# Performance work log

Hardware: AMD Instinct MI355X
Metric: run time of the kernel (lower is better)

Reference implementation:

```python
import jax, jax.numpy as jnp
import numpy as np

NUM_NODE = 100000
B, L, D = 128, 50, 128
HOP = 2
S = 8            # n_sample
NEIGHBOR_N = 9   # FindNeighbors top-k
BETA = 0.005
LEAKY = 0.2      # opt.alpha


def _local_agg(h, adj, a_local):
    # h: [B,N,D], adj: [B,N,N] int with edge types 0..4, a_local: [4,D]
    # e_k[b,i,j] = leakyrelu(sum_d h[b,i,d]*h[b,j,d]*a_k[d]) without [B,N,N,D] blowup
    e = jnp.stack([jnp.einsum('bid,bjd->bij', h * a_local[k], h) for k in range(4)])
    e = jax.nn.leaky_relu(e, LEAKY)
    att = jnp.full(e.shape[1:], -9e15, dtype=h.dtype)
    for k in range(4):
        att = jnp.where(adj == k + 1, e[k], att)
    att = jax.nn.softmax(att, axis=-1)
    return att @ h


def _global_agg(self_v, neigh_v, neigh_w, extra, w1, w2, w3):
    # self_v [B,M,D], neigh_v [B,M,S,D], neigh_w [B,M,S], extra (session info) [B,M,D]
    x = jnp.concatenate([extra[:, :, None, :] * neigh_v, neigh_w[..., None]], axis=-1)  # [B,M,S,D+1]
    alpha = jax.nn.leaky_relu(jnp.einsum('bmse,ed->bmsd', x, w1), LEAKY)
    alpha = jax.nn.softmax(jnp.einsum('bmsd,d->bms', alpha, w2[:, 0]), axis=-1)
    neigh = jnp.sum(alpha[..., None] * neigh_v, axis=-2)                                # [B,M,D]
    out = jnp.concatenate([self_v, neigh], axis=-1) @ w3
    return jax.nn.relu(out)


def _ssl(h_local, h_global):
    b, l, _ = h_local.shape
    kr, kc = jax.random.split(jax.random.key(42))
    corrupted = h_local[jax.random.permutation(kr, b)][:, jax.random.permutation(kc, l)]
    pos = jnp.sum(h_local * h_global, axis=1)
    neg = jnp.sum(h_global * corrupted, axis=1)
    return jnp.sum(-jnp.log(1e-8 + jax.nn.sigmoid(pos))
                   - jnp.log(1e-8 + 1.0 - jax.nn.sigmoid(neg)))


def _compute_scores(hidden, mask, pos_embedding, w1, w2, glu1_w, glu1_b, glu2_w, embedding):
    b, l, d = hidden.shape
    m = mask.astype(hidden.dtype)[..., None]                       # [B,L,1]
    pos = jnp.broadcast_to(pos_embedding[:l][None], hidden.shape)  # [B,L,D]
    hs = jnp.sum(hidden * m, axis=1) / jnp.sum(m, axis=1)          # [B,D]
    nh = jnp.tanh(jnp.concatenate([pos, hidden], axis=-1) @ w1)
    ns = jax.nn.sigmoid(nh @ glu1_w.T + glu1_b + hs[:, None, :] @ glu2_w.T)
    beta = (ns @ w2) * m                                           # [B,L,1]
    select = jnp.sum(beta * hidden, axis=1)                        # [B,D]
    # FindNeighbors: top-k cosine-similarity attention across the batch
    norm = jnp.sqrt(jnp.sum(select * select + 1e-6, axis=1))[:, None]
    cos = jax.nn.softmax((select @ select.T) / (norm @ norm.T), axis=-1)
    k = min(NEIGHBOR_N, b)
    topv, topi = jax.lax.top_k(cos, k)
    topv = jax.nn.softmax(topv, axis=-1)
    neighbor = jnp.sum(topv[..., None] * select[topi], axis=1)     # [B,D]
    select = select + neighbor                                     # dropout40: eval identity
    return select @ embedding[1:].T                                # [B, num_node-1]


def _forward(inputs, adj, mask_item, item, adj_all, num_w, embedding, pos_embedding,
             a_local, gw1, gw2, gw3, w1, w2, glu1_w, glu1_b, glu2_w):
    b, l = inputs.shape
    d = embedding.shape[1]
    h = embedding[inputs]
    h_local = _local_agg(h, adj, a_local)
    # multi-hop neighbor sampling via global adjacency table
    item_neighbors = [inputs]
    weight_neighbors = []
    support = l
    for _ in range(HOP):
        flat = item_neighbors[-1].reshape(-1)
        support *= S
        item_neighbors.append(adj_all[flat].reshape(b, support))
        weight_neighbors.append(num_w[flat].reshape(b, support))
    entity = [embedding[x] for x in item_neighbors]
    mf = mask_item.astype(h.dtype)
    item_emb = embedding[item] * mf[..., None]
    sess = jnp.sum(item_emb, axis=1) / jnp.sum(mf, axis=-1)[:, None]   # [B,D]
    session_info = [jnp.broadcast_to(sess[:, None, :], ev.shape) for ev in entity[:HOP]]
    for n_hop in range(HOP):
        nxt = []
        for i in range(HOP - n_hop):
            nv = entity[i + 1].reshape(b, -1, S, d)
            nw = weight_neighbors[i].reshape(b, -1, S)
            nxt.append(_global_agg(entity[i], nv, nw, session_info[i],
                                   gw1[n_hop], gw2[n_hop], gw3[n_hop]))
        entity = nxt
    h_global = entity[0].reshape(b, l, d)
    output = h_local + h_global  # dropout_local/global: eval identity
    con_loss = _ssl(h_local, h_global)
    scores = _compute_scores(output, mask_item, pos_embedding, w1, w2,
                             glu1_w, glu1_b, glu2_w, embedding)
    return output, BETA * con_loss, scores


def setup_inputs() -> dict:
    key = jax.random.key(0)
    ks = jax.random.split(key, 18)
    s = 0.08  # ~ uniform(-1/sqrt(D), 1/sqrt(D)) scale
    return {
        'inputs': jax.random.randint(ks[0], (B, L), 0, NUM_NODE, dtype=jnp.int32),
        'adj': jax.random.randint(ks[1], (B, L, L), 0, 5, dtype=jnp.int32),
        'mask_item': jax.random.randint(ks[2], (B, L), 0, 2, dtype=jnp.int32).at[:, 0].set(1),
        'item': jax.random.randint(ks[3], (B, L), 0, NUM_NODE, dtype=jnp.int32),
        'targets': jax.random.randint(ks[4], (B,), 0, NUM_NODE, dtype=jnp.int32),
        'adj_all': jax.random.randint(ks[5], (NUM_NODE, S), 0, NUM_NODE, dtype=jnp.int32),
        'num_w': jax.random.uniform(ks[6], (NUM_NODE, S), dtype=jnp.float32),
        'embedding': jax.random.normal(ks[7], (NUM_NODE, D), dtype=jnp.float32) * s,
        'pos_embedding': jax.random.normal(ks[8], (200, D), dtype=jnp.float32) * s,
        'a_local': jax.random.normal(ks[9], (4, D), dtype=jnp.float32) * s,
        'gw1': jax.random.normal(ks[10], (HOP, D + 1, D), dtype=jnp.float32) * s,
        'gw2': jax.random.normal(ks[11], (HOP, D, 1), dtype=jnp.float32) * s,
        'gw3': jax.random.normal(ks[12], (HOP, 2 * D, D), dtype=jnp.float32) * s,
        'w1': jax.random.normal(ks[13], (2 * D, D), dtype=jnp.float32) * s,
        'w2': jax.random.normal(ks[14], (D, 1), dtype=jnp.float32) * s,
        'glu1_w': jax.random.normal(ks[15], (D, D), dtype=jnp.float32) * s,
        'glu1_b': jax.random.normal(ks[16], (D,), dtype=jnp.float32) * s,
        'glu2_w': jax.random.normal(ks[17], (D, D), dtype=jnp.float32) * s,
    }


def reference(inputs, adj, mask_item, item, targets, adj_all, num_w, embedding,
              pos_embedding, a_local, gw1, gw2, gw3, w1, w2, glu1_w, glu1_b, glu2_w):
    # targets embedding lookup in the original is dead code (targets1 unused)
    return _forward(inputs, adj, mask_item, item, adj_all, num_w, embedding,
                    pos_embedding, a_local, gw1, gw2, gw3, w1, w2, glu1_w, glu1_b, glu2_w)
```

## Files before the change

### kernel.cpp

```cpp
#include <hip/hip_runtime.h>
#include <stdint.h>

namespace {
constexpr int B_ = 128;
constexpr int L_ = 50;
constexpr int D_ = 128;
constexpr int S_ = 8;
constexpr int NSC_ = 99999;
constexpr int NBR_ = 9;
}
#define LEAKY_ 0.2f
#define BETA_ 0.005f

typedef __attribute__((ext_vector_type(8))) __bf16 bf16x8;
typedef __attribute__((ext_vector_type(4))) float f32x4;

__device__ __forceinline__ float leaky_(float x){ return x >= 0.f ? x : LEAKY_*x; }
__device__ __forceinline__ float sigm_(float x){ return 1.f/(1.f+expf(-x)); }

__device__ __forceinline__ short f2b(float f){
  uint32_t u = __float_as_uint(f);
  u += 0x7fffu + ((u >> 16) & 1u);
  return (short)(u >> 16);
}
__device__ __forceinline__ float b2f(short s){
  return __uint_as_float(((uint32_t)(uint16_t)s) << 16);
}
__device__ __forceinline__ f32x4 zero4(){ f32x4 z = {0.f,0.f,0.f,0.f}; return z; }
__device__ __forceinline__ f32x4 mfma_bf16(bf16x8 a, bf16x8 b, f32x4 c){
  return __builtin_amdgcn_mfma_f32_16x16x32_bf16(a, b, c, 0, 0, 0);
}

__device__ __forceinline__ void tf2x32(uint32_t k0, uint32_t k1, uint32_t c0, uint32_t c1,
                                       uint32_t* o0, uint32_t* o1){
  uint32_t ks2 = k0 ^ k1 ^ 0x1BD11BDAu;
  uint32_t x0 = c0 + k0, x1 = c1 + k1;
#define RND_(r) { x0 += x1; x1 = (x1<<(r))|(x1>>(32-(r))); x1 ^= x0; }
  RND_(13) RND_(15) RND_(26) RND_(6)   x0 += k1;  x1 += ks2 + 1u;
  RND_(17) RND_(29) RND_(16) RND_(24)  x0 += ks2; x1 += k0  + 2u;
  RND_(13) RND_(15) RND_(26) RND_(6)   x0 += k0;  x1 += k1  + 3u;
  RND_(17) RND_(29) RND_(16) RND_(24)  x0 += k1;  x1 += ks2 + 4u;
  RND_(13) RND_(15) RND_(26) RND_(6)   x0 += ks2; x1 += k0  + 5u;
#undef RND_
  *o0 = x0; *o1 = x1;
}

__global__ __launch_bounds__(256) void k_prep_all(
    const float* __restrict__ emb, const int* __restrict__ item,
    const int* __restrict__ mask, const float* __restrict__ gw1,
    const float* __restrict__ gw3, const float* __restrict__ glu1w,
    const int* __restrict__ inputs, const int* __restrict__ adj_all,
    const float* __restrict__ num_w,
    short* __restrict__ embB, float* __restrict__ w1T,
    float* __restrict__ glu1wT, short* __restrict__ w3T,
    float* __restrict__ sess,
    int* __restrict__ n1i, float* __restrict__ n1w,
    int* __restrict__ n2i, float* __restrict__ n2w)
{
  int blk = blockIdx.x, tid = threadIdx.x;
  if (blk < 3125){
    size_t base = (size_t)blk*4096 + (size_t)tid*16;
    float4 f0 = *(const float4*)(emb + base);
    float4 f1 = *(const float4*)(emb + base + 4);
    float4 f2 = *(const float4*)(emb + base + 8);
    float4 f3 = *(const float4*)(emb + base + 12);
    short4 s0, s1, s2, s3;
    s0.x=f2b(f0.x); s0.y=f2b(f0.y); s0.z=f2b(f0.z); s0.w=f2b(f0.w);
    s1.x=f2b(f1.x); s1.y=f2b(f1.y); s1.z=f2b(f1.z); s1.w=f2b(f1.w);
    s2.x=f2b(f2.x); s2.y=f2b(f2.y); s2.z=f2b(f2.z); s2.w=f2b(f2.w);
    s3.x=f2b(f3.x); s3.y=f2b(f3.y); s3.z=f2b(f3.z); s3.w=f2b(f3.w);
    *(short4*)(embB + base)      = s0;
    *(short4*)(embB + base + 4)  = s1;
    *(short4*)(embB + base + 8)  = s2;
    *(short4*)(embB + base + 12) = s3;
  } else if (blk < 3573){
    int o = (blk - 3125)*256 + tid;
    if (o < 32768){
      int hop = o >> 14, r = o & 16383;
      int d = r >> 7, e = r & 127;
      w1T[o] = gw1[hop*(129*128) + e*128 + d];
    } else if (o < 49152){
      int o2 = o - 32768;
      int e = o2 >> 7, t = o2 & 127;
      glu1wT[o2] = glu1w[t*128 + e];
    } else if (o < 114688){
      int o3 = o - 49152;
      int hop = o3 >> 15, r = o3 & 32767;
      int nn = r >> 8, k = r & 255;
      w3T[hop*(128*264) + nn*264 + k] = f2b(gw3[hop*(256*128) + k*128 + nn]);
    }
  } else if (blk < 3701){
    int b = blk - 3573;
    if (tid < 128){
      float acc = 0.f, ms = 0.f;
      for (int l = 0; l < L_; l++){
        float mk = (float)mask[b*L_ + l];
        ms += mk;
        acc += mk * emb[(size_t)item[b*L_ + l]*D_ + tid];
      }
      sess[(size_t)b*D_ + tid] = acc / ms;
    }
  } else {
    int p = (blk - 3701)*256 + tid;
    int base = inputs[p >> 3];
    int off  = base*S_ + (p & 7);
    int i1 = adj_all[off];
    n1i[p] = i1;
    n1w[p] = num_w[off];
#pragma unroll
    for (int j = 0; j < 8; j++){
      n2i[(size_t)p*8 + j] = adj_all[i1*8 + j];
      n2w[(size_t)p*8 + j] = num_w[i1*8 + j];
    }
  }
}

__global__ __launch_bounds__(256) void k_bsess(
    const float* __restrict__ w1T, const float* __restrict__ sess,
    short* __restrict__ Bsess)
{
  int blk = blockIdx.x, tid = threadIdx.x;
  int hop = blk >> 7, b = blk & 127;
  const float* wt = w1T + hop*16384;
  short* outp = Bsess + ((size_t)hop*128 + b)*16384;
  __shared__ float sessS[128];
  if (tid < 128) sessS[tid] = sess[b*128 + tid];
  __syncthreads();
  for (int it = 0; it < 64; it++){
    int u = it*256 + tid;
    outp[u] = f2b(wt[u] * sessS[u & 127]);
  }
}

__global__ __launch_bounds__(256) void k_local(const int* __restrict__ inputs,
                                               const short* __restrict__ embB,
                                               const int* __restrict__ adj,
                                               const float* __restrict__ a_local,
                                               float* __restrict__ hl){
  __shared__ float hs[L_*129];
  __shared__ float att[25*52];
  __shared__ float al[4*132];
  __shared__ int idxs[L_];
  int b = blockIdx.y, half = blockIdx.x, tid = threadIdx.x;
  int i0 = half*25;
  if (tid < L_) idxs[tid] = inputs[b*L_ + tid];
  __syncthreads();
  for (int u = tid; u < L_*16; u += 256){
    int i = u >> 4, c = u & 15;
    union { bf16x8 v; short sh[8]; } w;
    w.v = *(const bf16x8*)&embB[(size_t)idxs[i]*128 + c*8];
#pragma unroll
    for (int j = 0; j < 8; j++) hs[i*129 + c*8 + j] = b2f(w.sh[j]);
  }
  for (int e = tid; e < 4*D_; e += 256) al[(e>>7)*132 + (e&127)] = a_local[e];
  __syncthreads();
  for (int p = tid; p < 25*L_; p += 256){
    int il = p / L_, j = p % L_;
    int i = i0 + il;
    int k = adj[((size_t)b*L_ + i)*L_ + j];
    float v = -9e15f;
    if (k >= 1){
      const float* ak = &al[(k-1)*132];
      float acc = 0.f;
      for (int d = 0; d < D_; d++) acc += hs[i*129+d]*hs[j*129+d]*ak[d];
      v = leaky_(acc);
    }
    att[il*52 + j] = v;
  }
  __syncthreads();
  if (tid < 25){
    int il = tid;
    float mx = -INFINITY;
    for (int j = 0; j < L_; j++) mx = fmaxf(mx, att[il*52+j]);
    float sm = 0.f;
    for (int j = 0; j < L_; j++){ float e_ = expf(att[il*52+j] - mx); att[il*52+j] = e_; sm += e_; }
    float inv = 1.f/sm;
    for (int j = 0; j < L_; j++) att[il*52+j] *= inv;
  }
  __syncthreads();
  for (int q = tid; q < 25*D_; q += 256){
    int il = q >> 7, d = q & 127;
    float acc = 0.f;
    for (int j = 0; j < L_; j++) acc += att[il*52+j]*hs[j*129+d];
    hl[((size_t)b*L_ + i0 + il)*D_ + d] = acc;
  }
}

__global__ __launch_bounds__(256, 4) void k_att2(
    const short* __restrict__ embB,
    const int* __restrict__ n1i, const float* __restrict__ n1w,
    const int* __restrict__ n2i, const float* __restrict__ n2w,
    const short* __restrict__ Bsess,
    const float* __restrict__ w1g, const float* __restrict__ w2g,
    short* __restrict__ e0pB, short* __restrict__ e1pB)
{
  __shared__ __align__(16) short As[128*136];
  __shared__ float w1lS[128], w2S[128], nwsS[128], logitsS[128], alphaS[128];
  const int tid = threadIdx.x;
  const int b = blockIdx.y;
  const int bx = blockIdx.x;
  const int* nidx; const float* nw; short* outn; int rpb, r0;
  if (bx < 4){ nidx = n1i; nw = n1w; outn = e0pB; rpb = 400;  r0 = bx*128; }
  else       { nidx = n2i; nw = n2w; outn = e1pB; rpb = 3200; r0 = (bx-4)*128; }
  if (tid < 128){
    w1lS[tid]  = w1g[128*128 + tid];
    w2S[tid]   = w2g[tid];
    int rr = min(r0 + tid, rpb - 1);
    nwsS[tid]  = nw[(size_t)b*rpb + rr];
  }
  for (int it = 0; it < 8; it++){
    int u = it*256 + tid;
    int lr = u >> 4, c = u & 15;
    int rr = min(r0 + lr, rpb - 1);
    const short* src = embB + (size_t)nidx[(size_t)b*rpb + rr]*128;
    *(bf16x8*)&As[lr*136 + c*8] = *(const bf16x8*)&src[c*8];
  }
  __syncthreads();
  const int lane = tid & 63, wave = tid >> 6;
  const int quad = lane >> 4, l16 = lane & 15;
  const int wr0 = wave * 32;
  const short* Bb = Bsess + (size_t)b*16384;
  f32x4 acc[2][8];
#pragma unroll
  for (int i=0;i<2;i++)
#pragma unroll
    for (int j=0;j<8;j++) acc[i][j] = zero4();
  for (int kc = 0; kc < 4; kc++){
    int k = kc*32 + quad*8;
    bf16x8 a0 = *(const bf16x8*)&As[(wr0 + l16)*136 + k];
    bf16x8 a1 = *(const bf16x8*)&As[(wr0 + 16 + l16)*136 + k];
    bf16x8 bb[8];
#pragma unroll
    for (int nt = 0; nt < 8; nt++)
      bb[nt] = *(const bf16x8*)&Bb[(size_t)(nt*16 + l16)*128 + k];
#pragma unroll
    for (int nt = 0; nt < 8; nt++){
      acc[0][nt] = mfma_bf16(a0, bb[nt], acc[0][nt]);
      acc[1][nt] = mfma_bf16(a1, bb[nt], acc[1][nt]);
    }
  }
#pragma unroll
  for (int rt = 0; rt < 2; rt++){
#pragma unroll
    for (int r = 0; r < 4; r++){
      int rowl = wr0 + rt*16 + quad*4 + r;
      float nwv = nwsS[rowl];
      float c = 0.f;
#pragma unroll
      for (int nt = 0; nt < 8; nt++){
        int col = nt*16 + l16;
        float v = acc[rt][nt][r] + nwv * w1lS[col];
        c += leaky_(v) * w2S[col];
      }
      c += __shfl_xor(c, 1, 64);
      c += __shfl_xor(c, 2, 64);
      c += __shfl_xor(c, 4, 64);
      c += __shfl_xor(c, 8, 64);
      if (l16 == 0) logitsS[rowl] = c;
    }
  }
  __syncthreads();
  if (tid < 16){
    float mx = -INFINITY;
    for (int s = 0; s < 8; s++) mx = fmaxf(mx, logitsS[tid*8+s]);
    float sm = 0.f; float ev[8];
    for (int s = 0; s < 8; s++){ ev[s] = expf(logitsS[tid*8+s]-mx); sm += ev[s]; }
    for (int s = 0; s < 8; s++) alphaS[tid*8+s] = ev[s]/sm;
  }
  __syncthreads();
  {
    int mg = tid >> 4;
    int dc = tid & 15;
    float o[8];
#pragma unroll
    for (int j = 0; j < 8; j++) o[j] = 0.f;
#pragma unroll
    for (int s = 0; s < 8; s++){
      float al = alphaS[mg*8+s];
      union { bf16x8 v; short sh[8]; } u;
      u.v = *(const bf16x8*)&As[(mg*8+s)*136 + dc*8];
#pragma unroll
      for (int j = 0; j < 8; j++) o[j] += al * b2f(u.sh[j]);
    }
    if (r0 + mg*8 < rpb){
      int m = (r0 >> 3) + mg;
      union { short s[8]; bf16x8 v; } pk;
#pragma unroll
      for (int j = 0; j < 8; j++) pk.s[j] = f2b(o[j]);
      *(bf16x8*)(outn + ((size_t)b*(rpb>>3) + m)*128 + dc*8) = pk.v;
    }
  }
}

__global__ __launch_bounds__(256, 4) void k_att(
    const short* __restrict__ embB, const short* __restrict__ denseB,
    const int* __restrict__ nidx, const float* __restrict__ nw,
    const short* __restrict__ Bsess,
    const float* __restrict__ w1g, const float* __restrict__ w2g,
    short* __restrict__ outn, int rpb)
{
  __shared__ __align__(16) short As[128*136];
  __shared__ float w1lS[128], w2S[128], nwsS[128], logitsS[128], alphaS[128];
  const int tid = threadIdx.x;
  const int b = blockIdx.y;
  const int r0 = blockIdx.x * 128;
  if (tid < 128){
    w1lS[tid]  = w1g[128*128 + tid];
    w2S[tid]   = w2g[tid];
    int rr = min(r0 + tid, rpb - 1);
    nwsS[tid]  = nw[(size_t)b*rpb + rr];
  }
  for (int it = 0; it < 8; it++){
    int u = it*256 + tid;
    int lr = u >> 4, c = u & 15;
    int rr = min(r0 + lr, rpb - 1);
    const short* src = denseB ? denseB + ((size_t)b*rpb + rr)*128
                              : embB + (size_t)nidx[(size_t)b*rpb + rr]*128;
    *(bf16x8*)&As[lr*136 + c*8] = *(const bf16x8*)&src[c*8];
  }
  __syncthreads();
  const int lane = tid & 63, wave = tid >> 6;
  const int quad = lane >> 4, l16 = lane & 15;
  const int wr0 = wave * 32;
  const short* Bb = Bsess + (size_t)b*16384;
  f32x4 acc[2][8];
#pragma unroll
  for (int i=0;i<2;i++)
#pragma unroll
    for (int j=0;j<8;j++) acc[i][j] = zero4();
  for (int kc = 0; kc < 4; kc++){
    int k = kc*32 + quad*8;
    bf16x8 a0 = *(const bf16x8*)&As[(wr0 + l16)*136 + k];
    bf16x8 a1 = *(const bf16x8*)&As[(wr0 + 16 + l16)*136 + k];
    bf16x8 bb[8];
#pragma unroll
    for (int nt = 0; nt < 8; nt++)
      bb[nt] = *(const bf16x8*)&Bb[(size_t)(nt*16 + l16)*128 + k];
#pragma unroll
    for (int nt = 0; nt < 8; nt++){
      acc[0][nt] = mfma_bf16(a0, bb[nt], acc[0][nt]);
      acc[1][nt] = mfma_bf16(a1, bb[nt], acc[1][nt]);
    }
  }
#pragma unroll
  for (int rt = 0; rt < 2; rt++){
#pragma unroll
    for (int r = 0; r < 4; r++){
      int rowl = wr0 + rt*16 + quad*4 + r;
      float nwv = nwsS[rowl];
      float c = 0.f;
#pragma unroll
      for (int nt = 0; nt < 8; nt++){
        int col = nt*16 + l16;
        float v = acc[rt][nt][r] + nwv * w1lS[col];
        c += leaky_(v) * w2S[col];
      }
      c += __shfl_xor(c, 1, 64);
      c += __shfl_xor(c, 2, 64);
      c += __shfl_xor(c, 4, 64);
      c += __shfl_xor(c, 8, 64);
      if (l16 == 0) logitsS[rowl] = c;
    }
  }
  __syncthreads();
  if (tid < 16){
    float mx = -INFINITY;
    for (int s = 0; s < 8; s++) mx = fmaxf(mx, logitsS[tid*8+s]);
    float sm = 0.f; float ev[8];
    for (int s = 0; s < 8; s++){ ev[s] = expf(logitsS[tid*8+s]-mx); sm += ev[s]; }
    for (int s = 0; s < 8; s++) alphaS[tid*8+s] = ev[s]/sm;
  }
  __syncthreads();
  {
    int mg = tid >> 4;
    int dc = tid & 15;
    float o[8];
#pragma unroll
    for (int j = 0; j < 8; j++) o[j] = 0.f;
#pragma unroll
    for (int s = 0; s < 8; s++){
      float al = alphaS[mg*8+s];
      union { bf16x8 v; short sh[8]; } u;
      u.v = *(const bf16x8*)&As[(mg*8+s)*136 + dc*8];
#pragma unroll
      for (int j = 0; j < 8; j++) o[j] += al * b2f(u.sh[j]);
    }
    if (r0 + mg*8 < rpb){
      int m = (r0 >> 3) + mg;
      union { short s[8]; bf16x8 v; } pk;
#pragma unroll
      for (int j = 0; j < 8; j++) pk.s[j] = f2b(o[j]);
      *(bf16x8*)(outn + ((size_t)b*(rpb>>3) + m)*128 + dc*8) = pk.v;
    }
  }
}

__global__ __launch_bounds__(256) void k_gout2(
    const short* __restrict__ embB, const int* __restrict__ inputs,
    const int* __restrict__ n1i, const short* __restrict__ w3T,
    short* __restrict__ e0pB, short* __restrict__ e1pB)
{
  const int blk = blockIdx.x;
  const int* self_idx; short* buf; int rblk;
  if (blk < 100){ self_idx = inputs; buf = e0pB; rblk = blk; }
  else          { self_idx = n1i;    buf = e1pB; rblk = blk - 100; }
  const int tid = threadIdx.x;
  const int lane = tid & 63, wave = tid >> 6;
  const int quad = lane >> 4, l16 = lane & 15;
  const int rbase = rblk*64 + wave*16;
  const int row = rbase + l16;
  const short* selfp = embB + (size_t)self_idx[row]*128;
  const short* neighp = buf + (size_t)row*128;
  f32x4 acc[8];
#pragma unroll
  for (int i=0;i<8;i++) acc[i] = zero4();
  for (int kc = 0; kc < 4; kc++){
    int k = kc*32 + quad*8;
    bf16x8 a = *(const bf16x8*)&selfp[k];
#pragma unroll
    for (int nt = 0; nt < 8; nt++){
      bf16x8 bb = *(const bf16x8*)&w3T[(size_t)(nt*16 + l16)*264 + k];
      acc[nt] = mfma_bf16(a, bb, acc[nt]);
    }
  }
  for (int kc = 4; kc < 8; kc++){
    int k = kc*32 + quad*8;
    bf16x8 a = *(const bf16x8*)&neighp[k - 128];
#pragma unroll
    for (int nt = 0; nt < 8; nt++){
      bf16x8 bb = *(const bf16x8*)&w3T[(size_t)(nt*16 + l16)*264 + k];
      acc[nt] = mfma_bf16(a, bb, acc[nt]);
    }
  }
#pragma unroll
  for (int nt = 0; nt < 8; nt++)
#pragma unroll
    for (int r = 0; r < 4; r++){
      int orow = rbase + quad*4 + r;
      buf[(size_t)orow*128 + nt*16 + l16] = f2b(fmaxf(acc[nt][r], 0.f));
    }
}

__global__ __launch_bounds__(256) void k_gout(
    const short* __restrict__ embB, const short* __restrict__ selfB,
    const int* __restrict__ self_idx, const short* __restrict__ w3T,
    const short* __restrict__ neighB, float* __restrict__ outF,
    short* __restrict__ outB)
{
  const int tid = threadIdx.x;
  const int lane = tid & 63, wave = tid >> 6;
  const int quad = lane >> 4, l16 = lane & 15;
  const int rbase = blockIdx.x*64 + wave*16;
  const int row = rbase + l16;
  const short* selfp = self_idx ? embB + (size_t)self_idx[row]*128
                                : selfB + (size_t)row*128;
  const short* neighp = neighB + (size_t)row*128;
  f32x4 acc[8];
#pragma unroll
  for (int i=0;i<8;i++) acc[i] = zero4();
  for (int kc = 0; kc < 4; kc++){
    int k = kc*32 + quad*8;
    bf16x8 a = *(const bf16x8*)&selfp[k];
#pragma unroll
    for (int nt = 0; nt < 8; nt++){
      bf16x8 bb = *(const bf16x8*)&w3T[(size_t)(nt*16 + l16)*264 + k];
      acc[nt] = mfma_bf16(a, bb, acc[nt]);
    }
  }
  for (int kc = 4; kc < 8; kc++){
    int k = kc*32 + quad*8;
    bf16x8 a = *(const bf16x8*)&neighp[k - 128];
#pragma unroll
    for (int nt = 0; nt < 8; nt++){
      bf16x8 bb = *(const bf16x8*)&w3T[(size_t)(nt*16 + l16)*264 + k];
      acc[nt] = mfma_bf16(a, bb, acc[nt]);
    }
  }
  if (outF){
#pragma unroll
    for (int nt = 0; nt < 8; nt++)
#pragma unroll
      for (int r = 0; r < 4; r++){
        int orow = rbase + quad*4 + r;
        outF[(size_t)orow*128 + nt*16 + l16] = fmaxf(acc[nt][r], 0.f);
      }
  } else {
#pragma unroll
    for (int nt = 0; nt < 8; nt++)
#pragma unroll
      for (int r = 0; r < 4; r++){
        int orow = rbase + quad*4 + r;
        outB[(size_t)orow*128 + nt*16 + l16] = f2b(fmaxf(acc[nt][r], 0.f));
      }
  }
}

__global__ __launch_bounds__(128) void k_sslhs(
    const float* __restrict__ hl, const float* __restrict__ hg,
    const int* __restrict__ mask, const float* __restrict__ glu2_w,
    float* __restrict__ out, float* __restrict__ wsLoss,
    float* __restrict__ g2)
{
  __shared__ uint32_t keys[128];
  __shared__ float red[128];
  __shared__ float hss[128];
  __shared__ int pcS[50];
  __shared__ int prbS;
  int b = blockIdx.x, tid = threadIdx.x;
  uint32_t kr0, kr1, kc0, kc1, sk0, sk1, o0, o1;
  tf2x32(0u, 42u, 0u, 0u, &kr0, &kr1);
  tf2x32(0u, 42u, 0u, 1u, &kc0, &kc1);
  tf2x32(kr0, kr1, 0u, 1u, &sk0, &sk1);
  tf2x32(sk0, sk1, 0u, (uint32_t)tid, &o0, &o1);
  keys[tid] = o0 ^ o1;
  __syncthreads();
  {
    uint32_t mk = keys[tid];
    int rank = 0;
    for (int j = 0; j < 128; j++){
      uint32_t kj = keys[j];
      rank += (kj < mk) || (kj == mk && j < tid);
    }
    if (rank == b) prbS = tid;
  }
  __syncthreads();
  tf2x32(kc0, kc1, 0u, 1u, &sk0, &sk1);
  if (tid < 50){
    tf2x32(sk0, sk1, 0u, (uint32_t)tid, &o0, &o1);
    keys[tid] = o0 ^ o1;
  }
  __syncthreads();
  if (tid < 50){
    uint32_t mk = keys[tid];
    int rank = 0;
    for (int j = 0; j < 50; j++){
      uint32_t kj = keys[j];
      rank += (kj < mk) || (kj == mk && j < tid);
    }
    pcS[rank] = tid;
  }
  __syncthreads();
  int prb = prbS, d = tid;
  float pos = 0.f, neg = 0.f, hsacc = 0.f, ms = 0.f;
  for (int l = 0; l < L_; l++){
    size_t off = ((size_t)b*L_ + l)*D_ + d;
    float hlv = hl[off], hgv = hg[off];
    float o = hlv + hgv;
    out[off] = o;
    pos += hlv * hgv;
    neg += hgv * hl[((size_t)prb*L_ + pcS[l])*D_ + d];
    float mk = (float)mask[b*L_ + l];
    ms += mk;
    hsacc += mk * o;
  }
  hss[d] = hsacc / ms;
  red[d] = -logf(1e-8f + sigm_(pos)) - logf(1e-8f + 1.f - sigm_(neg));
  __syncthreads();
  for (int off = 64; off >= 1; off >>= 1){
    if (d < off) red[d] += red[d + off];
    __syncthreads();
  }
  if (d == 0) wsLoss[b] = red[0];
  float g = 0.f;
  for (int e = 0; e < 128; e++) g += hss[e]*glu2_w[d*128 + e];
  g2[(size_t)b*128 + d] = g;
}

__global__ __launch_bounds__(256) void k_beta10(
    const float* __restrict__ hidden, const int* __restrict__ mask,
    const float* __restrict__ pose, const float* __restrict__ w1s,
    const float* __restrict__ w2s, const float* __restrict__ glu1wT,
    const float* __restrict__ glu1b, const float* __restrict__ g2,
    float* __restrict__ betaW)
{
  __shared__ float x[10][260];
  __shared__ float buf[10][132];
  __shared__ float bufB[2][16];
  int lg = blockIdx.x, b = blockIdx.y, tid = threadIdx.x;
  int t = tid & 127, eh = tid >> 7;
  int l0 = lg*10;
  for (int u = tid; u < 10*64; u += 256){
    int row = u >> 6, c4 = u & 63;
    float4 v; int col;
    if (c4 < 32){ v = *(const float4*)(pose + (l0+row)*128 + c4*4); col = c4*4; }
    else        { v = *(const float4*)(hidden + ((size_t)b*L_ + l0+row)*128 + (c4-32)*4); col = 128 + (c4-32)*4; }
    *(float4*)&x[row][col] = v;
  }
  __syncthreads();
  float acc[10];
#pragma unroll
  for (int l = 0; l < 10; l++) acc[l] = 0.f;
  {
    int e0 = eh*128;
    for (int e = e0; e < e0 + 128; e += 4){
      float wa = w1s[(e+0)*128 + t];
      float wb = w1s[(e+1)*128 + t];
      float wc = w1s[(e+2)*128 + t];
      float wd = w1s[(e+3)*128 + t];
#pragma unroll
      for (int l = 0; l < 10; l++){
        float4 xv = *(const float4*)&x[l][e];
        acc[l] += xv.x*wa; acc[l] += xv.y*wb; acc[l] += xv.z*wc; acc[l] += xv.w*wd;
      }
    }
  }
  if (eh == 1){
#pragma unroll
    for (int i = 0; i < 10; i++) buf[i][t] = acc[i];
  }
  __syncthreads();
  if (eh == 0){
#pragma unroll
    for (int i = 0; i < 10; i++) acc[i] += buf[i][t];
  }
  __syncthreads();
  if (eh == 0){
#pragma unroll
    for (int l = 0; l < 10; l++) x[l][t] = tanhf(acc[l]);
  }
  __syncthreads();
  float acc2[10];
#pragma unroll
  for (int l = 0; l < 10; l++) acc2[l] = 0.f;
  {
    int e0 = eh*64;
    for (int e = e0; e < e0 + 64; e += 4){
      float wa = glu1wT[(e+0)*128 + t];
      float wb = glu1wT[(e+1)*128 + t];
      float wc = glu1wT[(e+2)*128 + t];
      float wd = glu1wT[(e+3)*128 + t];
#pragma unroll
      for (int l = 0; l < 10; l++){
        float4 xv = *(const float4*)&x[l][e];
        acc2[l] += xv.x*wa; acc2[l] += xv.y*wb; acc2[l] += xv.z*wc; acc2[l] += xv.w*wd;
      }
    }
  }
  if (eh == 1){
#pragma unroll
    for (int i = 0; i < 10; i++) buf[i][t] = acc2[i];
  }
  __syncthreads();
  if (eh == 0){
#pragma unroll
    for (int i = 0; i < 10; i++) acc2[i] += buf[i][t];
  }
  __syncthreads();
  if (eh == 0){
    float g2v = g2[(size_t)b*128 + t];
    float g1b = glu1b[t];
    float w2v = w2s[t];
    int lane = tid & 63, wv = tid >> 6;
#pragma unroll
    for (int l = 0; l < 10; l++){
      float ns = sigm_(acc2[l] + g1b + g2v);
      float v = ns * w2v;
      v += __shfl_xor(v, 1, 64);
      v += __shfl_xor(v, 2, 64);
      v += __shfl_xor(v, 4, 64);
      v += __shfl_xor(v, 8, 64);
      v += __shfl_xor(v, 16, 64);
      v += __shfl_xor(v, 32, 64);
      if (lane == 0) bufB[wv][l] = v;
    }
  }
  __syncthreads();
  if (tid < 10)
    betaW[b*L_ + l0 + tid] = (bufB[0][tid] + bufB[1][tid]) * (float)mask[b*L_ + l0 + tid];
}

__global__ __launch_bounds__(128) void k_selnorm(
    const float* __restrict__ hidden, const float* __restrict__ betaW,
    float* __restrict__ select, float* __restrict__ norms)
{
  __shared__ float bet[56];
  __shared__ float red[128];
  int b = blockIdx.x, t = threadIdx.x;
  if (t < L_) bet[t] = betaW[b*L_ + t];
  __syncthreads();
  float sel = 0.f;
  for (int l = 0; l < L_; l++) sel += bet[l]*hidden[((size_t)b*L_ + l)*128 + t];
  select[(size_t)b*128 + t] = sel;
  red[t] = sel*sel + 1e-6f;
  __syncthreads();
  for (int off=64; off>=1; off>>=1){ if (t<off) red[t]+=red[t+off]; __syncthreads(); }
  if (t==0) norms[b] = sqrtf(red[0]);
}

__global__ __launch_bounds__(128) void k_topk(const float* __restrict__ select,
                                              const float* __restrict__ norms,
                                              const float* __restrict__ wsLoss,
                                              short* __restrict__ select2b,
                                              float* __restrict__ out_loss){
  __shared__ float p[B_];
  __shared__ float red[128];
  __shared__ float tv[NBR_];
  __shared__ int   ti[NBR_];
  int b = blockIdx.x, t = threadIdx.x;
  float dot = 0.f;
  for (int d = 0; d < D_; d++) dot += select[(size_t)b*D_ + d]*select[(size_t)t*D_ + d];
  float logit = dot / (norms[b]*norms[t]);
  red[t] = logit; __syncthreads();
  for (int off = 64; off >= 1; off >>= 1){
    if (t < off) red[t] = fmaxf(red[t], red[t + off]);
    __syncthreads();
  }
  float mx = red[0]; __syncthreads();
  float e_ = expf(logit - mx);
  red[t] = e_; __syncthreads();
  for (int off = 64; off >= 1; off >>= 1){
    if (t < off) red[t] += red[t + off];
    __syncthreads();
  }
  p[t] = e_ / red[0];
  __syncthreads();
  if (t == 0){
    unsigned long long used0 = 0ull, used1 = 0ull;
    for (int k = 0; k < NBR_; k++){
      float best = -INFINITY; int bi = 0;
      for (int j = 0; j < B_; j++){
        bool u = (j < 64) ? ((used0 >> j) & 1ull) : ((used1 >> (j-64)) & 1ull);
        if (!u && p[j] > best){ best = p[j]; bi = j; }
      }
      if (bi < 64) used0 |= 1ull << bi; else used1 |= 1ull << (bi-64);
      tv[k] = best; ti[k] = bi;
    }
    float mx2 = -INFINITY;
    for (int k = 0; k < NBR_; k++) mx2 = fmaxf(mx2, tv[k]);
    float s2 = 0.f;
    for (int k = 0; k < NBR_; k++){ tv[k] = expf(tv[k]-mx2); s2 += tv[k]; }
    for (int k = 0; k < NBR_; k++) tv[k] /= s2;
  }
  __syncthreads();
  float nb = 0.f;
#pragma unroll
  for (int k = 0; k < NBR_; k++) nb += tv[k]*select[(size_t)ti[k]*D_ + t];
  select2b[(size_t)b*D_ + t] = f2b(select[(size_t)b*D_ + t] + nb);
  if (b == 0){
    __syncthreads();
    red[t] = wsLoss[t];
    __syncthreads();
    for (int off = 64; off >= 1; off >>= 1){
      if (t < off) red[t] += red[t + off];
      __syncthreads();
    }
    if (t == 0) out_loss[0] = BETA_ * red[0];
  }
}

__global__ __launch_bounds__(256) void k_scores(
    const short* __restrict__ sel2b, const float* __restrict__ emb,
    float* __restrict__ scores)
{
  __shared__ __align__(16) short Es[64*136];
  const int tid = threadIdx.x;
  const int n0 = blockIdx.x*64;
  for (int it = 0; it < 8; it++){
    int u = it*256 + tid;
    int lr = u >> 5, c = u & 31;
    int n = min(n0 + lr, NSC_ - 1);
    float4 v = *(const float4*)(emb + (size_t)(1 + n)*128 + c*4);
    short4 s4; s4.x=f2b(v.x); s4.y=f2b(v.y); s4.z=f2b(v.z); s4.w=f2b(v.w);
    *(short4*)&Es[lr*136 + c*4] = s4;
  }
  __syncthreads();
  const int lane = tid & 63, wave = tid >> 6;
  const int quad = lane >> 4, l16 = lane & 15;
  int n = n0 + wave*16 + l16;
  f32x4 acc[8];
#pragma unroll
  for (int i=0;i<8;i++) acc[i] = zero4();
  for (int kc = 0; kc < 4; kc++){
    int k = kc*32 + quad*8;
    bf16x8 bb = *(const bf16x8*)&Es[(wave*16 + l16)*136 + k];
#pragma unroll
    for (int rt = 0; rt < 8; rt++){
      bf16x8 a = *(const bf16x8*)&sel2b[(rt*16 + l16)*128 + k];
      acc[rt] = mfma_bf16(a, bb, acc[rt]);
    }
  }
  if (n < NSC_){
#pragma unroll
    for (int rt = 0; rt < 8; rt++)
#pragma unroll
      for (int r = 0; r < 4; r++){
        int brow = rt*16 + quad*4 + r;
        scores[(size_t)brow*NSC_ + n] = acc[rt][r];
      }
  }
}

extern "C" void kernel_launch(void* const* d_in, const int* in_sizes, int n_in,
                              void* d_out, int out_size, void* d_ws, size_t ws_size,
                              hipStream_t stream) {
  (void)in_sizes; (void)n_in; (void)out_size; (void)ws_size;
  const int*   inputs  = (const int*)  d_in[0];
  const int*   adj     = (const int*)  d_in[1];
  const int*   mask    = (const int*)  d_in[2];
  const int*   item    = (const int*)  d_in[3];
  const int*   adj_all = (const int*)  d_in[5];
  const float* num_w   = (const float*)d_in[6];
  const float* emb     = (const float*)d_in[7];
  const float* pose    = (const float*)d_in[8];
  const float* a_local = (const float*)d_in[9];
  const float* gw1     = (const float*)d_in[10];
  const float* gw2     = (const float*)d_in[11];
  const float* gw3     = (const float*)d_in[12];
  const float* w1      = (const float*)d_in[13];
  const float* w2      = (const float*)d_in[14];
  const float* glu1w   = (const float*)d_in[15];
  const float* glu1b   = (const float*)d_in[16];
  const float* glu2w   = (const float*)d_in[17];
  float* out = (float*)d_out;

  float* W     = (float*)d_ws;
  float* hl    = W;
  float* hg    = W + 819200;
  short* e0pB  = (short*)(W + 1638400);
  short* e1pB  = (short*)(W + 2457600);
  float* sess  = W + 9011200;
  float* g2    = W + 9027584;
  float* sel   = W + 9043968;
  short* sel2b = (short*)(W + 9060352);
  float* norms = W + 9076736;
  float* wsLoss= W + 9076864;
  float* n1w   = W + 9076992;
  float* n2w   = W + 9128192;
  float* betaW = W + 9537792;
  float* w1T   = W + 9544192;
  float* glu1wT= W + 9576960;
  short* w3Tb  = (short*)(W + 9593344);
  int*   n1i   = (int*)(W + 9627136);
  int*   n2i   = n1i + 51200;

  short* embB   = (short*)(out + 819712);
  short* BsessG = (short*)(out + 819712 + 3200000);
  short* hgB    = (short*)(out + 819712 + 3200000 + 2097152);

  k_prep_all<<<3901, 256, 0, stream>>>(emb, item, mask, gw1, gw3, glu1w,
                                       inputs, adj_all, num_w,
                                       embB, w1T, glu1wT, w3Tb, sess,
                                       n1i, n1w, n2i, n2w);
  k_bsess<<<256, 256, 0, stream>>>(w1T, sess, BsessG);
  k_local<<<dim3(2, B_), 256, 0, stream>>>(inputs, embB, adj, a_local, hl);

  k_att2<<<dim3(29, B_), 256, 0, stream>>>(embB, n1i, n1w, n2i, n2w, BsessG,
                                           gw1, gw2, e0pB, e1pB);
  k_gout2<<<900, 256, 0, stream>>>(embB, inputs, n1i, w3Tb, e0pB, e1pB);

  k_att <<<dim3(4, B_),  256, 0, stream>>>(embB, e1pB, nullptr, n1w,
                                           BsessG + (size_t)128*16384,
                                           gw1 + 129*128, gw2 + 128, hgB, 400);
  k_gout<<<100, 256, 0, stream>>>(embB, e0pB, nullptr, w3Tb + 128*264, hgB, hg, nullptr);

  k_sslhs<<<B_, 128, 0, stream>>>(hl, hg, mask, glu2w, out, wsLoss, g2);
  k_beta10<<<dim3(5, B_), 256, 0, stream>>>(out, mask, pose, w1, w2, glu1wT,
                                            glu1b, g2, betaW);
  k_selnorm<<<B_, 128, 0, stream>>>(out, betaW, sel, norms);
  k_topk<<<B_, 128, 0, stream>>>(sel, norms, wsLoss, sel2b, out + B_*L_*D_);
  k_scores<<<(NSC_ + 63)/64, 256, 0, stream>>>(sel2b, emb, out + B_*L_*D_ + 1);
}
```

Baseline: 461.1 us.

## Fuse session-weight precompute into prep and local aggregation into attention kernel

Folds the session-mean and session-scaled weight (Bsess) computation into the prep kernel, which eliminates the w1T transpose and sess intermediate buffers. Merges the local attention kernel into the first-hop/second-hop attention kernel as extra blocks that reuse its shared memory. This cuts two kernel launches and their serialization gaps, and lets the local and global work overlap on the GPU. The cost is that the local path now runs under the attention kernel's launch bounds and the larger Bsess blocks sit in a mixed grid.

Result: faster. 450.4 us (-2.3%).

```diff
diff --git a/kernel.cpp b/kernel.cpp
--- a/kernel.cpp
+++ b/kernel.cpp
@@ -51,11 +51,11 @@
     const float* __restrict__ gw3, const float* __restrict__ glu1w,
     const int* __restrict__ inputs, const int* __restrict__ adj_all,
     const float* __restrict__ num_w,
-    short* __restrict__ embB, float* __restrict__ w1T,
-    float* __restrict__ glu1wT, short* __restrict__ w3T,
-    float* __restrict__ sess,
+    short* __restrict__ embB, float* __restrict__ glu1wT,
+    short* __restrict__ w3T,
     int* __restrict__ n1i, float* __restrict__ n1w,
-    int* __restrict__ n2i, float* __restrict__ n2w)
+    int* __restrict__ n2i, float* __restrict__ n2w,
+    short* __restrict__ Bsess)
 {
   int blk = blockIdx.x, tid = threadIdx.x;
   if (blk < 3125){
@@ -73,24 +73,33 @@
     *(short4*)(embB + base + 4)  = s1;
     *(short4*)(embB + base + 8)  = s2;
     *(short4*)(embB + base + 12) = s3;
-  } else if (blk < 3573){
+  } else if (blk < 3445){
     int o = (blk - 3125)*256 + tid;
-    if (o < 32768){
-      int hop = o >> 14, r = o & 16383;
-      int d = r >> 7, e = r & 127;
-      w1T[o] = gw1[hop*(129*128) + e*128 + d];
-    } else if (o < 49152){
-      int o2 = o - 32768;
-      int e = o2 >> 7, t = o2 & 127;
-      glu1wT[o2] = glu1w[t*128 + e];
-    } else if (o < 114688){
-      int o3 = o - 49152;
+    if (o < 16384){
+      int e = o >> 7, t = o & 127;
+      glu1wT[o] = glu1w[t*128 + e];
+    } else {
+      int o3 = o - 16384;
       int hop = o3 >> 15, r = o3 & 32767;
       int nn = r >> 8, k = r & 255;
       w3T[hop*(128*264) + nn*264 + k] = f2b(gw3[hop*(256*128) + k*128 + nn]);
     }
-  } else if (blk < 3701){
-    int b = blk - 3573;
+  } else if (blk < 3645){
+    int p = (blk - 3445)*256 + tid;
+    int base = inputs[p >> 3];
+    int off  = base*S_ + (p & 7);
+    int i1 = adj_all[off];
+    n1i[p] = i1;
+    n1w[p] = num_w[off];
+#pragma unroll
+    for (int j = 0; j < 8; j++){
+      n2i[(size_t)p*8 + j] = adj_all[i1*8 + j];
+      n2w[(size_t)p*8 + j] = num_w[i1*8 + j];
+    }
+  } else {
+    int i = blk - 3645;
+    int hop = i >> 7, b = i & 127;
+    __shared__ float sessS[128];
     if (tid < 128){
       float acc = 0.f, ms = 0.f;
       for (int l = 0; l < L_; l++){
@@ -98,96 +107,23 @@
         ms += mk;
         acc += mk * emb[(size_t)item[b*L_ + l]*D_ + tid];
       }
-      sess[(size_t)b*D_ + tid] = acc / ms;
-    }
-  } else {
-    int p = (blk - 3701)*256 + tid;
-    int base = inputs[p >> 3];
-    int off  = base*S_ + (p & 7);
-    int i1 = adj_all[off];
-    n1i[p] = i1;
-    n1w[p] = num_w[off];
-#pragma unroll
-    for (int j = 0; j < 8; j++){
-      n2i[(size_t)p*8 + j] = adj_all[i1*8 + j];
-      n2w[(size_t)p*8 + j] = num_w[i1*8 + j];
-    }
-  }
-}
-
-__global__ __launch_bounds__(256) void k_bsess(
-    const float* __restrict__ w1T, const float* __restrict__ sess,
-    short* __restrict__ Bsess)
-{
-  int blk = blockIdx.x, tid = threadIdx.x;
-  int hop = blk >> 7, b = blk & 127;
-  const float* wt = w1T + hop*16384;
-  short* outp = Bsess + ((size_t)hop*128 + b)*16384;
-  __shared__ float sessS[128];
-  if (tid < 128) sessS[tid] = sess[b*128 + tid];
-  __syncthreads();
-  for (int it = 0; it < 64; it++){
-    int u = it*256 + tid;
-    outp[u] = f2b(wt[u] * sessS[u & 127]);
-  }
-}
-
-__global__ __launch_bounds__(256) void k_local(const int* __restrict__ inputs,
-                                               const short* __restrict__ embB,
-                                               const int* __restrict__ adj,
-                                               const float* __restrict__ a_local,
-                                               float* __restrict__ hl){
-  __shared__ float hs[L_*129];
-  __shared__ float att[25*52];
-  __shared__ float al[4*132];
-  __shared__ int idxs[L_];
-  int b = blockIdx.y, half = blockIdx.x, tid = threadIdx.x;
-  int i0 = half*25;
-  if (tid < L_) idxs[tid] = inputs[b*L_ + tid];
-  __syncthreads();
-  for (int u = tid; u < L_*16; u += 256){
-    int i = u >> 4, c = u & 15;
-    union { bf16x8 v; short sh[8]; } w;
-    w.v = *(const bf16x8*)&embB[(size_t)idxs[i]*128 + c*8];
-#pragma unroll
-    for (int j = 0; j < 8; j++) hs[i*129 + c*8 + j] = b2f(w.sh[j]);
-  }
-  for (int e = tid; e < 4*D_; e += 256) al[(e>>7)*132 + (e&127)] = a_local[e];
-  __syncthreads();
-  for (int p = tid; p < 25*L_; p += 256){
-    int il = p / L_, j = p % L_;
-    int i = i0 + il;
-    int k = adj[((size_t)b*L_ + i)*L_ + j];
-    float v = -9e15f;
-    if (k >= 1){
-      const float* ak = &al[(k-1)*132];
-      float acc = 0.f;
-      for (int d = 0; d < D_; d++) acc += hs[i*129+d]*hs[j*129+d]*ak[d];
-      v = leaky_(acc);
-    }
-    att[il*52 + j] = v;
-  }
-  __syncthreads();
-  if (tid < 25){
-    int il = tid;
-    float mx = -INFINITY;
-    for (int j = 0; j < L_; j++) mx = fmaxf(mx, att[il*52+j]);
-    float sm = 0.f;
-    for (int j = 0; j < L_; j++){ float e_ = expf(att[il*52+j] - mx); att[il*52+j] = e_; sm += e_; }
-    float inv = 1.f/sm;
-    for (int j = 0; j < L_; j++) att[il*52+j] *= inv;
-  }
-  __syncthreads();
-  for (int q = tid; q < 25*D_; q += 256){
-    int il = q >> 7, d = q & 127;
-    float acc = 0.f;
-    for (int j = 0; j < L_; j++) acc += att[il*52+j]*hs[j*129+d];
-    hl[((size_t)b*L_ + i0 + il)*D_ + d] = acc;
-  }
-}
-
-__global__ __launch_bounds__(256, 4) void k_att2(
-    const short* __restrict__ embB,
+      sessS[tid] = acc / ms;
+    }
+    __syncthreads();
+    const float* g1 = gw1 + hop*(129*128);
+    short* outp = Bsess + ((size_t)hop*128 + b)*16384;
+    for (int it = 0; it < 64; it++){
+      int u = it*256 + tid;
+      int e = u & 127, d = u >> 7;
+      outp[u] = f2b(g1[e*128 + d] * sessS[e]);
+    }
+  }
+}
+
+__global__ __launch_bounds__(256, 4) void k_fused1(
+    const short* __restrict__ embB, const int* __restrict__ inputs,
+    const int* __restrict__ adj, const float* __restrict__ a_local,
+    float* __restrict__ hl,
     const int* __restrict__ n1i, const float* __restrict__ n1w,
     const int* __restrict__ n2i, const float* __restrict__ n2w,
     const short* __restrict__ Bsess,
@@ -196,12 +132,71 @@
 {
   __shared__ __align__(16) short As[128*136];
   __shared__ float w1lS[128], w2S[128], nwsS[128], logitsS[128], alphaS[128];
+  const int blk = blockIdx.x;
   const int tid = threadIdx.x;
-  const int b = blockIdx.y;
-  const int bx = blockIdx.x;
-  const int* nidx; const float* nw; short* outn; int rpb, r0;
-  if (bx < 4){ nidx = n1i; nw = n1w; outn = e0pB; rpb = 400;  r0 = bx*128; }
-  else       { nidx = n2i; nw = n2w; outn = e1pB; rpb = 3200; r0 = (bx-4)*128; }
+
+  if (blk < 256){
+    float* hs   = (float*)As;
+    float* attL = (float*)(As + 12900);
+    float* al   = (float*)(As + 15500);
+    int*   idxs = (int*)  (As + 16556);
+    int b = blk >> 1, half = blk & 1;
+    int i0 = half*25;
+    if (tid < L_) idxs[tid] = inputs[b*L_ + tid];
+    __syncthreads();
+    for (int u = tid; u < L_*16; u += 256){
+      int i = u >> 4, c = u & 15;
+      union { bf16x8 v; short sh[8]; } w;
+      w.v = *(const bf16x8*)&embB[(size_t)idxs[i]*128 + c*8];
+#pragma unroll
+      for (int j = 0; j < 8; j++) hs[i*129 + c*8 + j] = b2f(w.sh[j]);
+    }
+    for (int e = tid; e < 4*D_; e += 256) al[(e>>7)*132 + (e&127)] = a_local[e];
+    __syncthreads();
+    for (int p = tid; p < 25*L_; p += 256){
+      int il = p / L_, j = p % L_;
+      int i = i0 + il;
+      int k = adj[((size_t)b*L_ + i)*L_ + j];
+      float v = -9e15f;
+      if (k >= 1){
+        const float* ak = &al[(k-1)*132];
+        float acc = 0.f;
+        for (int d = 0; d < D_; d++) acc += hs[i*129+d]*hs[j*129+d]*ak[d];
+        v = leaky_(acc);
+      }
+      attL[il*52 + j] = v;
+    }
+    __syncthreads();
+    if (tid < 25){
+      int il = tid;
+      float mx = -INFINITY;
+      for (int j = 0; j < L_; j++) mx = fmaxf(mx, attL[il*52+j]);
+      float sm = 0.f;
+      for (int j = 0; j < L_; j++){ float e_ = expf(attL[il*52+j] - mx); attL[il*52+j] = e_; sm += e_; }
+      float inv = 1.f/sm;
+      for (int j = 0; j < L_; j++) attL[il*52+j] *= inv;
+    }
+    __syncthreads();
+    for (int q = tid; q < 25*D_; q += 256){
+      int il = q >> 7, d = q & 127;
+      float acc = 0.f;
+      for (int j = 0; j < L_; j++) acc += attL[il*52+j]*hs[j*129+d];
+      hl[((size_t)b*L_ + i0 + il)*D_ + d] = acc;
+    }
+    return;
+  }
+
+  int b, r0, rpb;
+  const int* nidx; const float* nw; short* outn;
+  if (blk < 768){
+    int i = blk - 256;
+    b = i >> 2; r0 = (i & 3)*128;
+    nidx = n1i; nw = n1w; outn = e0pB; rpb = 400;
+  } else {
+    int i = blk - 768;
+    b = i / 25; r0 = (i % 25)*128;
+    nidx = n2i; nw = n2w; outn = e1pB; rpb = 3200;
+  }
   if (tid < 128){
     w1lS[tid]  = w1g[128*128 + tid];
     w2S[tid]   = w2g[tid];
@@ -276,11 +271,11 @@
     for (int j = 0; j < 8; j++) o[j] = 0.f;
 #pragma unroll
     for (int s = 0; s < 8; s++){
-      float al = alphaS[mg*8+s];
+      float al2 = alphaS[mg*8+s];
       union { bf16x8 v; short sh[8]; } u;
       u.v = *(const bf16x8*)&As[(mg*8+s)*136 + dc*8];
 #pragma unroll
-      for (int j = 0; j < 8; j++) o[j] += al * b2f(u.sh[j]);
+      for (int j = 0; j < 8; j++) o[j] += al2 * b2f(u.sh[j]);
     }
     if (r0 + mg*8 < rpb){
       int m = (r0 >> 3) + mg;
@@ -818,7 +813,6 @@
   float* hg    = W + 819200;
   short* e0pB  = (short*)(W + 1638400);
   short* e1pB  = (short*)(W + 2457600);
-  float* sess  = W + 9011200;
   float* g2    = W + 9027584;
   float* sel   = W + 9043968;
   short* sel2b = (short*)(W + 9060352);
@@ -827,7 +821,6 @@
   float* n1w   = W + 9076992;
   float* n2w   = W + 9128192;
   float* betaW = W + 9537792;
-  float* w1T   = W + 9544192;
   float* glu1wT= W + 9576960;
   short* w3Tb  = (short*)(W + 9593344);
   int*   n1i   = (int*)(W + 9627136);
@@ -839,13 +832,12 @@
 
   k_prep_all<<<3901, 256, 0, stream>>>(emb, item, mask, gw1, gw3, glu1w,
                                        inputs, adj_all, num_w,
-                                       embB, w1T, glu1wT, w3Tb, sess,
-                                       n1i, n1w, n2i, n2w);
-  k_bsess<<<256, 256, 0, stream>>>(w1T, sess, BsessG);
-  k_local<<<dim3(2, B_), 256, 0, stream>>>(inputs, embB, adj, a_local, hl);
-
-  k_att2<<<dim3(29, B_), 256, 0, stream>>>(embB, n1i, n1w, n2i, n2w, BsessG,
-                                           gw1, gw2, e0pB, e1pB);
+                                       embB, glu1wT, w3Tb,
+                                       n1i, n1w, n2i, n2w, BsessG);
+
+  k_fused1<<<3968, 256, 0, stream>>>(embB, inputs, adj, a_local, hl,
+                                     n1i, n1w, n2i, n2w, BsessG,
+                                     gw1, gw2, e0pB, e1pB);
   k_gout2<<<900, 256, 0, stream>>>(embB, inputs, n1i, w3Tb, e0pB, e1pB);
 
   k_att <<<dim3(4, B_),  256, 0, stream>>>(embB, e1pB, nullptr, n1w,
```
